# Performance work log

Hardware: AMD Instinct MI355X
Metric: run time of the kernel (lower is better)

The kernel has to match this reference:

```python
import jax, jax.numpy as jnp
import numpy as np

D_MODEL = 1024
NHEAD = 16


def unitnorm(v):
    # F.normalize(v, dim=-1): v / max(||v||_2, 1e-12)
    n = jnp.sqrt(jnp.sum(v * v, axis=-1, keepdims=True))
    return v / jnp.maximum(n, 1e-12)


def setup_inputs() -> dict:
    key = jax.random.key(0)
    ks = jax.random.split(key, 14)
    d = D_MODEL
    sc = 1.0 / np.sqrt(d)
    inp = jax.random.normal(ks[0], (2048, 8, d), dtype=jnp.float32)
    def lin(kw, kb, out_dim):
        W = jax.random.uniform(kw, (out_dim, d), minval=-sc, maxval=sc, dtype=jnp.float32)
        b = jax.random.uniform(kb, (out_dim,), minval=-sc, maxval=sc, dtype=jnp.float32)
        return W, b
    Wq_w, Wq_b = lin(ks[1], ks[2], d)
    Wk_w, Wk_b = lin(ks[3], ks[4], d)
    Wv_w, Wv_b = lin(ks[5], ks[6], d)
    Wo_w, Wo_b = lin(ks[7], ks[8], d)
    Ww_w, Ww_b = lin(ks[9], ks[10], NHEAD)
    Wr_w, Wr_b = lin(ks[11], ks[12], NHEAD)
    return {"inp": inp, "Wq_w": Wq_w, "Wq_b": Wq_b, "Wk_w": Wk_w, "Wk_b": Wk_b,
            "Wv_w": Wv_w, "Wv_b": Wv_b, "Wo_w": Wo_w, "Wo_b": Wo_b,
            "Ww_w": Ww_w, "Ww_b": Ww_b, "Wr_w": Wr_w, "Wr_b": Wr_b}


def reference(inp, Wq_w, Wq_b, Wk_w, Wk_b, Wv_w, Wv_b, Wo_w, Wo_b, Ww_w, Ww_b, Wr_w, Wr_b):
    src = inp  # src=None path
    S, B, d = inp.shape
    n = NHEAD
    # torch Linear: x @ W.T + b
    k = (src @ Wk_w.T + Wk_b).reshape(S, B, n, -1)
    v = (src @ Wv_w.T + Wv_b).reshape(S, B, n, -1)
    q = (inp @ Wq_w.T + Wq_b).reshape(S, B, n, -1)
    k = unitnorm(k)
    q = unitnorm(q)
    w = jax.nn.sigmoid(src @ Ww_w.T + Ww_b)            # [S,B,n]
    A = jnp.einsum('sbnq,sbnv->bnvq', k, v * w[:, :, :, None])
    r = jax.nn.sigmoid(inp @ Wr_w.T + Wr_b)            # [S,B,n]
    out = jnp.einsum('sbnq,bnvq->sbnv', q, A) * r[:, :, :, None]
    out = out.reshape(S, B, d)
    out = out @ Wo_w.T + Wo_b
    return (out, A)
```

## Files before the change

### kernel.cpp

```cpp
#include <hip/hip_runtime.h>
#include <cstdint>
#include <cstddef>


typedef __bf16 bf16x8 __attribute__((ext_vector_type(8)));
typedef float  f32x4  __attribute__((ext_vector_type(4)));
typedef unsigned short u16x8 __attribute__((ext_vector_type(8)));
typedef unsigned short u16x4 __attribute__((ext_vector_type(4)));

#define ROWS 16384
#define DM   1024

__device__ __forceinline__ unsigned short f2bf(float f) {
  unsigned int u = __builtin_bit_cast(unsigned int, f);
  u += 0x7FFFu + ((u >> 16) & 1u);
  return (unsigned short)(u >> 16);
}
__device__ __forceinline__ float bf2f(unsigned short h) {
  unsigned int u = ((unsigned int)h) << 16;
  return __builtin_bit_cast(float, u);
}
__device__ __forceinline__ float sigm(float x) { return 1.0f / (1.0f + __expf(-x)); }

__device__ __forceinline__ void gload_lds16(const void* g, void* l) {
  __builtin_amdgcn_global_load_lds((__attribute__((address_space(1))) void*)(g),
                                   (__attribute__((address_space(3))) void*)(l),
                                   16, 0, 0);
}

__global__ __launch_bounds__(256) void k_cast_x(const float* __restrict__ X,
                                                unsigned short* __restrict__ Xb) {
  size_t i = ((size_t)blockIdx.x * 256 + threadIdx.x) * 8;
  f32x4 a = *(const f32x4*)(X + i);
  f32x4 b = *(const f32x4*)(X + i + 4);
  u16x8 o;
  o[0] = f2bf(a[0]); o[1] = f2bf(a[1]); o[2] = f2bf(a[2]); o[3] = f2bf(a[3]);
  o[4] = f2bf(b[0]); o[5] = f2bf(b[1]); o[6] = f2bf(b[2]); o[7] = f2bf(b[3]);
  *(u16x8*)(Xb + i) = o;
}

__global__ __launch_bounds__(256) void k_pack_w(
    const float* __restrict__ Wq, const float* __restrict__ Wk, const float* __restrict__ Wv,
    const float* __restrict__ Wo, const float* __restrict__ Ww, const float* __restrict__ Wr,
    const float* __restrict__ bq, const float* __restrict__ bk, const float* __restrict__ bv,
    const float* __restrict__ bw, const float* __restrict__ br,
    unsigned short* __restrict__ Wpack, float* __restrict__ biasP,
    unsigned short* __restrict__ WRw, float* __restrict__ biasWR,
    unsigned short* __restrict__ Wob) {
  int r = blockIdx.x, t = threadIdx.x;
  const float* src; float bias = 0.0f; unsigned short* dst; float* bdst;
  if (r < 1024)      { src = Wq + (size_t)r * DM;          bias = bq[r];        dst = Wpack + (size_t)r * DM;          bdst = biasP + r; }
  else if (r < 2048) { src = Wk + (size_t)(r - 1024) * DM; bias = bk[r - 1024]; dst = Wpack + (size_t)r * DM;          bdst = biasP + r; }
  else if (r < 3072) { src = Wv + (size_t)(r - 2048) * DM; bias = bv[r - 2048]; dst = Wpack + (size_t)r * DM;          bdst = biasP + r; }
  else if (r < 3088) { src = Ww + (size_t)(r - 3072) * DM; bias = bw[r - 3072]; dst = WRw + (size_t)(r - 3072) * DM;   bdst = biasWR + (r - 3072); }
  else if (r < 3104) { src = Wr + (size_t)(r - 3088) * DM; bias = br[r - 3088]; dst = WRw + (size_t)(r - 3072) * DM;   bdst = biasWR + (r - 3072); }
  else               { src = Wo + (size_t)(r - 3104) * DM;                      dst = Wob + (size_t)(r - 3104) * DM;   bdst = nullptr; }
  int c = t * 4;
  f32x4 v = *(const f32x4*)(src + c);
  u16x4 o;
  o[0] = f2bf(v[0]); o[1] = f2bf(v[1]); o[2] = f2bf(v[2]); o[3] = f2bf(v[3]);
  *(u16x4*)(dst + c) = o;
  if (t == 0 && bdst) *bdst = bias;
}

__global__ __launch_bounds__(256) void k_wr(const unsigned short* __restrict__ Xb,
                                            const unsigned short* __restrict__ WRw,
                                            const float* __restrict__ biasWR,
                                            float* __restrict__ WRf) {
  __shared__ __bf16 sA[128 * 64];
  __shared__ __bf16 sB[32 * 64];
  int t = threadIdx.x, lane = t & 63, wid = t >> 6;
  int m0 = blockIdx.x * 128;
  int l15 = lane & 15, l4 = lane >> 4;
  f32x4 acc[2][2];
#pragma unroll
  for (int i = 0; i < 2; ++i)
#pragma unroll
    for (int j = 0; j < 2; ++j) acc[i][j] = (f32x4){0.f, 0.f, 0.f, 0.f};
  int srow = t >> 3, schunk = (t & 7) * 8;
  for (int kt = 0; kt < DM; kt += 64) {
#pragma unroll
    for (int c = 0; c < 4; ++c)
      gload_lds16(Xb + (size_t)(m0 + c * 32 + srow) * DM + kt + schunk,
                  (void*)(sA + c * 2048 + wid * 512));
    gload_lds16(WRw + (size_t)srow * DM + kt + schunk, (void*)(sB + wid * 512));
    __syncthreads();
#pragma unroll
    for (int ks = 0; ks < 2; ++ks) {
      bf16x8 fa[2], fb[2];
#pragma unroll
      for (int mi = 0; mi < 2; ++mi)
        fa[mi] = *(const bf16x8*)(sA + (wid * 32 + mi * 16 + l15) * 64 + (ks * 4 + l4) * 8);
#pragma unroll
      for (int ni = 0; ni < 2; ++ni)
        fb[ni] = *(const bf16x8*)(sB + (ni * 16 + l15) * 64 + (ks * 4 + l4) * 8);
#pragma unroll
      for (int mi = 0; mi < 2; ++mi)
#pragma unroll
        for (int ni = 0; ni < 2; ++ni)
          acc[mi][ni] = __builtin_amdgcn_mfma_f32_16x16x32_bf16(fa[mi], fb[ni], acc[mi][ni], 0, 0, 0);
    }
    __syncthreads();
  }
#pragma unroll
  for (int mi = 0; mi < 2; ++mi)
#pragma unroll
    for (int e = 0; e < 4; ++e) {
      int row = m0 + wid * 32 + mi * 16 + 4 * l4 + e;
#pragma unroll
      for (int ni = 0; ni < 2; ++ni)
        WRf[(size_t)row * 32 + ni * 16 + l15] = acc[mi][ni][e] + biasWR[ni * 16 + l15];
    }
}


#define VMW(N)  asm volatile("s_waitcnt vmcnt(" #N ")" ::: "memory")
#define LGKM(N) asm volatile("s_waitcnt lgkmcnt(" #N ")" ::: "memory")
#define SB0     __builtin_amdgcn_sched_barrier(0)

__device__ __forceinline__ void stageT(const unsigned short* __restrict__ Asrc,
                                       const unsigned short* __restrict__ Bsrc,
                                       int kt, __bf16* sm, int sb, int w) {
#pragma unroll
  for (int c = 0; c < 2; ++c)
    gload_lds16(Asrc + (size_t)c * 128 * DM + kt, (void*)(sm + sb + c * 4096 + w * 512));
#pragma unroll
  for (int c = 0; c < 2; ++c)
    gload_lds16(Bsrc + (size_t)c * 128 * DM + kt, (void*)(sm + sb + 8192 + c * 4096 + w * 512));
}

__device__ __forceinline__ void rdFA(bf16x8 (&fa)[8], const __bf16* base, const int (&aoff)[8]) {
#pragma unroll
  for (int mi = 0; mi < 8; ++mi) fa[mi] = *(const bf16x8*)(base + aoff[mi]);
}
__device__ __forceinline__ void rdFB(bf16x8 (&fb)[4], const __bf16* base, const int (&boff)[4]) {
#pragma unroll
  for (int ni = 0; ni < 4; ++ni) fb[ni] = *(const bf16x8*)(base + boff[ni]);
}

#define MFMA32(FB)                                                                   \
  do {                                                                               \
    __builtin_amdgcn_s_setprio(1);                                                   \
    _Pragma("unroll") for (int mi = 0; mi < 8; ++mi)                                 \
    _Pragma("unroll") for (int ni = 0; ni < 4; ++ni)                                 \
      acc[mi][ni] = __builtin_amdgcn_mfma_f32_16x16x32_bf16(fa[mi], FB[ni],          \
                                                            acc[mi][ni], 0, 0, 0);  \
    __builtin_amdgcn_s_setprio(0);                                                   \
    SB0;                                                                             \
  } while (0)

__device__ __forceinline__ void gemm_d4(const unsigned short* __restrict__ Ag,
                                        const unsigned short* __restrict__ Bg,
                                        __bf16* sm, f32x4 (&acc)[8][4],
                                        int m0, int n0, int lane, int w) {
  const int wm = w >> 2, wn = w & 3;
  const int l15 = lane & 15, l4 = lane >> 4;
  const int t = w * 64 + lane;
  const int srow = t >> 2;
  const int schunk = ((t & 3) ^ ((srow >> 1) & 3)) * 8;
  const unsigned short* Asrc = Ag + (size_t)(m0 + srow) * DM + schunk;
  const unsigned short* Bsrc = Bg + (size_t)(n0 + srow) * DM + schunk;

  int aoff[8], boff[4];
#pragma unroll
  for (int mi = 0; mi < 8; ++mi) {
    int r = wm * 128 + mi * 16 + l15;
    aoff[mi] = r * 32 + ((l4 ^ ((r >> 1) & 3)) << 3);
  }
#pragma unroll
  for (int ni = 0; ni < 4; ++ni) {
    int r = wn * 64 + ni * 16 + l15;
    boff[ni] = 8192 + r * 32 + ((l4 ^ ((r >> 1) & 3)) << 3);
  }

  bf16x8 fa[8], fbA[4], fbB[4];
  stageT(Asrc, Bsrc, 0,  sm, 0,     w);
  stageT(Asrc, Bsrc, 32, sm, 16384, w);
  stageT(Asrc, Bsrc, 64, sm, 32768, w);
  VMW(8);
  __builtin_amdgcn_s_barrier(); SB0;
  rdFB(fbA, sm, boff);
  rdFA(fa, sm, aoff);
  VMW(4);
  __builtin_amdgcn_s_barrier(); SB0;

  int sb = 49152;
  int rb = 16384;
  for (int i = 0; i < 14; ++i) {
    stageT(Asrc, Bsrc, (2 * i + 3) * 32, sm, sb, w); sb = (sb + 16384) & 65535;
    rdFB(fbB, sm + rb, boff);
    LGKM(4); SB0;
    MFMA32(fbA);
    rdFA(fa, sm + rb, aoff); rb = (rb + 16384) & 65535;
    VMW(4);
    __builtin_amdgcn_s_barrier(); SB0;
    stageT(Asrc, Bsrc, (2 * i + 4) * 32, sm, sb, w); sb = (sb + 16384) & 65535;
    rdFB(fbA, sm + rb, boff);
    LGKM(4); SB0;
    MFMA32(fbB);
    rdFA(fa, sm + rb, aoff); rb = (rb + 16384) & 65535;
    VMW(4);
    __builtin_amdgcn_s_barrier(); SB0;
  }
  stageT(Asrc, Bsrc, 992, sm, sb, w);
  rdFB(fbB, sm + rb, boff);
  LGKM(4); SB0;
  MFMA32(fbA);
  rdFA(fa, sm + rb, aoff); rb = (rb + 16384) & 65535;
  VMW(4);
  __builtin_amdgcn_s_barrier(); SB0;
  rdFB(fbA, sm + rb, boff);
  LGKM(4); SB0;
  MFMA32(fbB);
  rdFA(fa, sm + rb, aoff); rb = (rb + 16384) & 65535;
  VMW(0);
  __builtin_amdgcn_s_barrier(); SB0;
  rdFB(fbB, sm + rb, boff);
  LGKM(4); SB0;
  MFMA32(fbA);
  rdFA(fa, sm + rb, aoff);
  LGKM(0); SB0;
  MFMA32(fbB);
}

__global__ __launch_bounds__(512, 2) void k_gemm_qkv6(
    const unsigned short* __restrict__ Xb, const unsigned short* __restrict__ Wpack,
    const float* __restrict__ biasP, const float* __restrict__ WRf,
    unsigned short* __restrict__ Qb, unsigned short* __restrict__ Kb,
    unsigned short* __restrict__ Vb) {
  __shared__ __bf16 sm[65536];
  const int t = threadIdx.x, lane = t & 63, w = t >> 6;
  const int wm = w >> 2, wn = w & 3;
  const int l15 = lane & 15, l4 = lane >> 4;
  int orig = blockIdx.x;
  int wg = (orig & 7) * 96 + (orig >> 3);
  const int m0 = (wg & 63) << 8;
  const int n0 = (wg >> 6) << 8;
  f32x4 acc[8][4];
#pragma unroll
  for (int i = 0; i < 8; ++i)
#pragma unroll
    for (int j = 0; j < 4; ++j) acc[i][j] = (f32x4){0.f, 0.f, 0.f, 0.f};
  gemm_d4(Xb, Wpack, sm, acc, m0, n0, lane, w);

  const int colbase = n0 + wn * 64;
  float bb[4];
#pragma unroll
  for (int ni = 0; ni < 4; ++ni) bb[ni] = biasP[colbase + ni * 16 + l15];

  if (colbase < 2048) {
    unsigned short* dstp = (colbase < 1024) ? Qb : Kb;
    int coff = (colbase < 1024) ? colbase : (colbase - 1024);
#pragma unroll
    for (int mi = 0; mi < 8; ++mi)
#pragma unroll
      for (int e = 0; e < 4; ++e) {
        float v[4]; float ssq = 0.f;
#pragma unroll
        for (int ni = 0; ni < 4; ++ni) { v[ni] = acc[mi][ni][e] + bb[ni]; ssq += v[ni] * v[ni]; }
        ssq += __shfl_xor(ssq, 1);
        ssq += __shfl_xor(ssq, 2);
        ssq += __shfl_xor(ssq, 4);
        ssq += __shfl_xor(ssq, 8);
        float sc = 1.0f / fmaxf(sqrtf(ssq), 1e-12f);
        int row = m0 + wm * 128 + mi * 16 + 4 * l4 + e;
#pragma unroll
        for (int ni = 0; ni < 4; ++ni)
          dstp[(size_t)row * DM + coff + ni * 16 + l15] = f2bf(v[ni] * sc);
      }
  } else {
    int hv = (colbase - 2048) >> 6;
    int coff = colbase - 2048;
#pragma unroll
    for (int mi = 0; mi < 8; ++mi)
#pragma unroll
      for (int e = 0; e < 4; ++e) {
        int row = m0 + wm * 128 + mi * 16 + 4 * l4 + e;
        float wgt = sigm(WRf[(size_t)row * 32 + hv]);
#pragma unroll
        for (int ni = 0; ni < 4; ++ni)
          Vb[(size_t)row * DM + coff + ni * 16 + l15] = f2bf((acc[mi][ni][e] + bb[ni]) * wgt);
      }
  }
}

__global__ __launch_bounds__(512, 2) void k_gemm_out6(
    const unsigned short* __restrict__ Ob, const unsigned short* __restrict__ Wob,
    const float* __restrict__ bo, float* __restrict__ Out) {
  __shared__ __bf16 sm[65536];
  const int t = threadIdx.x, lane = t & 63, w = t >> 6;
  const int wm = w >> 2, wn = w & 3;
  const int l15 = lane & 15, l4 = lane >> 4;
  int orig = blockIdx.x;
  int wg = (orig & 7) * 32 + (orig >> 3);
  const int m0 = (wg & 63) << 8;
  const int n0 = (wg >> 6) << 8;
  f32x4 acc[8][4];
#pragma unroll
  for (int i = 0; i < 8; ++i)
#pragma unroll
    for (int j = 0; j < 4; ++j) acc[i][j] = (f32x4){0.f, 0.f, 0.f, 0.f};
  gemm_d4(Ob, Wob, sm, acc, m0, n0, lane, w);

  float bb[4];
#pragma unroll
  for (int ni = 0; ni < 4; ++ni) bb[ni] = bo[n0 + wn * 64 + ni * 16 + l15];
#pragma unroll
  for (int mi = 0; mi < 8; ++mi)
#pragma unroll
    for (int e = 0; e < 4; ++e) {
      int row = m0 + wm * 128 + mi * 16 + 4 * l4 + e;
#pragma unroll
      for (int ni = 0; ni < 4; ++ni) {
        int col = n0 + wn * 64 + ni * 16 + l15;
        Out[(size_t)row * DM + col] = acc[mi][ni][e] + bb[ni];
      }
    }
}

__global__ __launch_bounds__(256, 2) void k_gemm_A(const unsigned short* __restrict__ Kb,
                                                   const unsigned short* __restrict__ Vb,
                                                   float* __restrict__ Apart) {
  __shared__ __bf16 sK[64 * 64];
  __shared__ __bf16 sV[64 * 64];
  int t = threadIdx.x, lane = t & 63, wid = t >> 6;
  int bn = blockIdx.x & 127, sk = blockIdx.x >> 7;
  int b = bn >> 4, n = bn & 15;
  f32x4 acc[4];
#pragma unroll
  for (int j = 0; j < 4; j++) acc[j] = (f32x4){0.f, 0.f, 0.f, 0.f};
  int lrow = lane >> 3, lcol = (lane & 7) * 8;

  for (int st = sk * 1024; st < (sk + 1) * 1024; st += 64) {
#pragma unroll
    for (int c = 0; c < 2; c++) {
      int r0 = wid * 16 + c * 8;
      size_t g = ((size_t)(st + r0 + lrow) * 8 + b) * DM + n * 64 + lcol;
      gload_lds16(Kb + g, (void*)(sK + r0 * 64));
      gload_lds16(Vb + g, (void*)(sV + r0 * 64));
    }
    __syncthreads();
#pragma unroll
    for (int kk = 0; kk < 64; kk += 32) {
      bf16x8 av, bv[4];
#pragma unroll
      for (int e = 0; e < 8; e++)
        av[e] = sV[(kk + 8 * (lane >> 4) + e) * 64 + wid * 16 + (lane & 15)];
#pragma unroll
      for (int jn = 0; jn < 4; jn++)
#pragma unroll
        for (int e = 0; e < 8; e++)
          bv[jn][e] = sK[(kk + 8 * (lane >> 4) + e) * 64 + jn * 16 + (lane & 15)];
#pragma unroll
      for (int jn = 0; jn < 4; jn++)
        acc[jn] = __builtin_amdgcn_mfma_f32_16x16x32_bf16(av, bv[jn], acc[jn], 0, 0, 0);
    }
    __syncthreads();
  }
  float* Ap = Apart + (size_t)(sk * 128 + bn) * 4096;
#pragma unroll
  for (int jn = 0; jn < 4; jn++) {
#pragma unroll
    for (int e = 0; e < 4; e++) {
      int i = wid * 16 + 4 * (lane >> 4) + e;
      int j = jn * 16 + (lane & 15);
      Ap[i * 64 + j] = acc[jn][e];
    }
  }
}

__global__ __launch_bounds__(256) void k_reduceA(const float* __restrict__ Apart,
                                                 float* __restrict__ Aout,
                                                 unsigned short* __restrict__ Abf) {
  int bn = blockIdx.x, t = threadIdx.x;
  size_t base = (size_t)bn * 4096 + t * 16;
#pragma unroll
  for (int j = 0; j < 4; ++j) {
    f32x4 x = *(const f32x4*)(Apart + base + j * 4);
    f32x4 y = *(const f32x4*)(Apart + (size_t)128 * 4096 + base + j * 4);
    x += y;
    *(f32x4*)(Aout + base + j * 4) = x;
    u16x4 o;
    o[0] = f2bf(x[0]); o[1] = f2bf(x[1]); o[2] = f2bf(x[2]); o[3] = f2bf(x[3]);
    *(u16x4*)(Abf + base + j * 4) = o;
  }
}

__global__ __launch_bounds__(256, 2) void k_gemm_o2(const unsigned short* __restrict__ Qb,
                                                    const unsigned short* __restrict__ Abf,
                                                    const float* __restrict__ WRf,
                                                    unsigned short* __restrict__ Ob) {
  __shared__ __bf16 sQ[128 * 64];
  __shared__ __bf16 sA[64 * 64];
  int t = threadIdx.x, lane = t & 63, wid = t >> 6;
  int bn = blockIdx.x & 127, stile = blockIdx.x >> 7;
  int b = bn >> 4, n = bn & 15;
  int s0 = stile * 128;
  int lrow = lane >> 3, lcol = (lane & 7) * 8;
#pragma unroll
  for (int c = 0; c < 4; c++) {
    int r0 = wid * 32 + c * 8;
    gload_lds16(Qb + ((size_t)(s0 + r0 + lrow) * 8 + b) * DM + n * 64 + lcol,
                (void*)(sQ + r0 * 64));
  }
#pragma unroll
  for (int c = 0; c < 2; c++) {
    int r0 = wid * 16 + c * 8;
    gload_lds16(Abf + (size_t)bn * 4096 + (size_t)(r0 + lrow) * 64 + lcol,
                (void*)(sA + r0 * 64));
  }
  __syncthreads();
  f32x4 acc[2][4];
#pragma unroll
  for (int i = 0; i < 2; i++)
#pragma unroll
    for (int j = 0; j < 4; j++) acc[i][j] = (f32x4){0.f, 0.f, 0.f, 0.f};
#pragma unroll
  for (int kk = 0; kk < 64; kk += 32) {
    bf16x8 aq[2], bA[4];
#pragma unroll
    for (int mi = 0; mi < 2; mi++)
      aq[mi] = *(const bf16x8*)(sQ + (wid * 32 + mi * 16 + (lane & 15)) * 64 + kk + 8 * (lane >> 4));
#pragma unroll
    for (int ni = 0; ni < 4; ni++)
      bA[ni] = *(const bf16x8*)(sA + (ni * 16 + (lane & 15)) * 64 + kk + 8 * (lane >> 4));
#pragma unroll
    for (int mi = 0; mi < 2; mi++)
#pragma unroll
      for (int ni = 0; ni < 4; ni++)
        acc[mi][ni] = __builtin_amdgcn_mfma_f32_16x16x32_bf16(aq[mi], bA[ni], acc[mi][ni], 0, 0, 0);
  }
#pragma unroll
  for (int mi = 0; mi < 2; mi++) {
#pragma unroll
    for (int e = 0; e < 4; e++) {
      int srow = wid * 32 + mi * 16 + 4 * (lane >> 4) + e;
      size_t row = (size_t)(s0 + srow) * 8 + b;
      float rv = sigm(WRf[row * 32 + 16 + n]);
#pragma unroll
      for (int ni = 0; ni < 4; ni++)
        Ob[row * DM + n * 64 + ni * 16 + (lane & 15)] = f2bf(acc[mi][ni][e] * rv);
    }
  }
}

extern "C" void kernel_launch(void* const* d_in, const int* in_sizes, int n_in,
                              void* d_out, int out_size, void* d_ws, size_t ws_size,
                              hipStream_t stream) {
  (void)in_sizes; (void)n_in; (void)out_size; (void)ws_size;
  const float* X  = (const float*)d_in[0];
  const float* Wq = (const float*)d_in[1];  const float* bq = (const float*)d_in[2];
  const float* Wk = (const float*)d_in[3];  const float* bk = (const float*)d_in[4];
  const float* Wv = (const float*)d_in[5];  const float* bv = (const float*)d_in[6];
  const float* Wo = (const float*)d_in[7];  const float* bo = (const float*)d_in[8];
  const float* Ww = (const float*)d_in[9];  const float* bw = (const float*)d_in[10];
  const float* Wr = (const float*)d_in[11]; const float* br = (const float*)d_in[12];

  char* ws = (char*)d_ws;
  unsigned short* Wpack = (unsigned short*)(ws + 0);
  float*          Apart = (float*)(ws + 0);
  unsigned short* Abf   = (unsigned short*)(ws + 4194304);
  float*          biasP = (float*)(ws + 6291456);
  unsigned short* WRw   = (unsigned short*)(ws + 6303744);
  float*          biasWR= (float*)(ws + 6369280);
  unsigned short* Wob   = (unsigned short*)(ws + 6369408);
  unsigned short* Xb    = (unsigned short*)(ws + 8466560);
  unsigned short* Ob    = Xb;
  unsigned short* Qb    = (unsigned short*)(ws + 42020992);
  unsigned short* Kb    = (unsigned short*)(ws + 75575424);
  unsigned short* Vb    = (unsigned short*)(ws + 109129856);
  float*          WRf   = (float*)(ws + 142684288);

  float* Out0 = (float*)d_out;
  float* Aout = Out0 + (size_t)ROWS * DM;

  k_cast_x<<<dim3(8192), dim3(256), 0, stream>>>(X, Xb);
  k_pack_w<<<dim3(4128), dim3(256), 0, stream>>>(Wq, Wk, Wv, Wo, Ww, Wr,
                                                 bq, bk, bv, bw, br,
                                                 Wpack, biasP, WRw, biasWR, Wob);
  k_wr<<<dim3(128), dim3(256), 0, stream>>>(Xb, WRw, biasWR, WRf);
  k_gemm_qkv6<<<dim3(768), dim3(512), 0, stream>>>(Xb, Wpack, biasP, WRf, Qb, Kb, Vb);
  k_gemm_A<<<dim3(256), dim3(256), 0, stream>>>(Kb, Vb, Apart);
  k_reduceA<<<dim3(128), dim3(256), 0, stream>>>(Apart, Aout, Abf);
  k_gemm_o2<<<dim3(2048), dim3(256), 0, stream>>>(Qb, Abf, WRf, Ob);
  k_gemm_out6<<<dim3(256), dim3(512), 0, stream>>>(Ob, Wob, bo, Out0);
}
```

Before: 241.9 us.

## Fuse X cast into k_wr, replace QKV GEMM pipeline, add nontemporal stores

Removes the separate fp32-to-bf16 cast kernel. k_wr now reads fp32 X directly, converts it, writes Xb to global and stages it into LDS for its own GEMM. Replaces the hand-pipelined QKV GEMM (gemm_d4 with explicit waitcnt scheduling) with a simpler double-buffered 64-wide K loop that uses XOR-swizzled LDS layout. Switches output stores in several kernels to nontemporal. This saves a launch and one pass over X, but k_wr runs only 128 blocks and now carries the whole cast, and the simpler GEMM loop may overlap loads with compute less well than the tuned one.

```diff
diff --git a/kernel.cpp b/kernel.cpp
--- a/kernel.cpp
+++ b/kernel.cpp
@@ -26,17 +26,6 @@
   __builtin_amdgcn_global_load_lds((__attribute__((address_space(1))) void*)(g),
                                    (__attribute__((address_space(3))) void*)(l),
                                    16, 0, 0);
-}
-
-__global__ __launch_bounds__(256) void k_cast_x(const float* __restrict__ X,
-                                                unsigned short* __restrict__ Xb) {
-  size_t i = ((size_t)blockIdx.x * 256 + threadIdx.x) * 8;
-  f32x4 a = *(const f32x4*)(X + i);
-  f32x4 b = *(const f32x4*)(X + i + 4);
-  u16x8 o;
-  o[0] = f2bf(a[0]); o[1] = f2bf(a[1]); o[2] = f2bf(a[2]); o[3] = f2bf(a[3]);
-  o[4] = f2bf(b[0]); o[5] = f2bf(b[1]); o[6] = f2bf(b[2]); o[7] = f2bf(b[3]);
-  *(u16x8*)(Xb + i) = o;
 }
 
 __global__ __launch_bounds__(256) void k_pack_w(
@@ -63,9 +52,10 @@
   if (t == 0 && bdst) *bdst = bias;
 }
 
-__global__ __launch_bounds__(256) void k_wr(const unsigned short* __restrict__ Xb,
+__global__ __launch_bounds__(256) void k_wr(const float* __restrict__ X,
                                             const unsigned short* __restrict__ WRw,
                                             const float* __restrict__ biasWR,
+                                            unsigned short* __restrict__ Xb,
                                             float* __restrict__ WRf) {
   __shared__ __bf16 sA[128 * 64];
   __shared__ __bf16 sB[32 * 64];
@@ -78,12 +68,24 @@
 #pragma unroll
     for (int j = 0; j < 2; ++j) acc[i][j] = (f32x4){0.f, 0.f, 0.f, 0.f};
   int srow = t >> 3, schunk = (t & 7) * 8;
+  int xr = t >> 1, xc = (t & 1) * 32;
   for (int kt = 0; kt < DM; kt += 64) {
-#pragma unroll
-    for (int c = 0; c < 4; ++c)
-      gload_lds16(Xb + (size_t)(m0 + c * 32 + srow) * DM + kt + schunk,
-                  (void*)(sA + c * 2048 + wid * 512));
     gload_lds16(WRw + (size_t)srow * DM + kt + schunk, (void*)(sB + wid * 512));
+    const float* xsrc = X + (size_t)(m0 + xr) * DM + kt + xc;
+    f32x4 xv[8];
+#pragma unroll
+    for (int j = 0; j < 8; ++j) xv[j] = *(const f32x4*)(xsrc + j * 4);
+    u16x8 o[4];
+#pragma unroll
+    for (int j = 0; j < 4; ++j) {
+#pragma unroll
+      for (int e = 0; e < 4; ++e) {
+        o[j][e]     = f2bf(xv[2 * j][e]);
+        o[j][e + 4] = f2bf(xv[2 * j + 1][e]);
+      }
+      *(u16x8*)(Xb + (size_t)(m0 + xr) * DM + kt + xc + j * 8) = o[j];
+      *(u16x8*)((unsigned short*)(sA + xr * 64 + xc) + j * 8) = o[j];
+    }
     __syncthreads();
 #pragma unroll
     for (int ks = 0; ks < 2; ++ks) {
@@ -113,6 +115,110 @@
     }
 }
 
+__global__ __launch_bounds__(512, 2) void k_gemm_qkv7(
+    const unsigned short* __restrict__ Xb, const unsigned short* __restrict__ Wpack,
+    const float* __restrict__ biasP, const float* __restrict__ WRf,
+    unsigned short* __restrict__ Qb, unsigned short* __restrict__ Kb,
+    unsigned short* __restrict__ Vb) {
+  __shared__ __bf16 sm[65536];
+  const int t = threadIdx.x, lane = t & 63, w = t >> 6;
+  const int wm = w >> 2, wn = w & 3;
+  const int l15 = lane & 15, l4 = lane >> 4, l7 = lane & 7;
+  int orig = blockIdx.x;
+  int wg = (orig & 7) * 96 + (orig >> 3);
+  const int m0 = (wg & 63) << 8;
+  const int n0 = (wg >> 6) << 8;
+
+  const int srow = t >> 3;
+  const int schunk = ((t & 7) ^ (srow & 7)) * 8;
+  const unsigned short* Asrc = Xb + (size_t)(m0 + srow) * DM + schunk;
+  const unsigned short* Bsrc = Wpack + (size_t)(n0 + srow) * DM + schunk;
+
+  f32x4 acc[8][4];
+#pragma unroll
+  for (int i = 0; i < 8; ++i)
+#pragma unroll
+    for (int j = 0; j < 4; ++j) acc[i][j] = (f32x4){0.f, 0.f, 0.f, 0.f};
+
+#define STAGE256(P, kt)                                                            \
+  do {                                                                             \
+    _Pragma("unroll") for (int c = 0; c < 4; ++c)                                  \
+      gload_lds16(Asrc + (size_t)c * 64 * DM + (kt),                               \
+                  (void*)(sm + (P) * 32768 + c * 4096 + w * 512));                 \
+    _Pragma("unroll") for (int c = 0; c < 4; ++c)                                  \
+      gload_lds16(Bsrc + (size_t)c * 64 * DM + (kt),                               \
+                  (void*)(sm + (P) * 32768 + 16384 + c * 4096 + w * 512));         \
+  } while (0)
+
+  STAGE256(0, 0);
+  __syncthreads();
+  for (int kt16 = 0; kt16 < 16; ++kt16) {
+    int P = kt16 & 1;
+    if (kt16 < 15) STAGE256(P ^ 1, (kt16 + 1) * 64);
+    const __bf16* A0 = sm + P * 32768;
+    const __bf16* B0 = A0 + 16384;
+#pragma unroll
+    for (int ks = 0; ks < 2; ++ks) {
+      bf16x8 fa[8], fb[4];
+      int ck = (((ks * 4 + l4) ^ l7) << 3);
+#pragma unroll
+      for (int mi = 0; mi < 8; ++mi)
+        fa[mi] = *(const bf16x8*)(A0 + (wm * 128 + mi * 16 + l15) * 64 + ck);
+#pragma unroll
+      for (int ni = 0; ni < 4; ++ni)
+        fb[ni] = *(const bf16x8*)(B0 + (wn * 64 + ni * 16 + l15) * 64 + ck);
+#pragma unroll
+      for (int mi = 0; mi < 8; ++mi)
+#pragma unroll
+        for (int ni = 0; ni < 4; ++ni)
+          acc[mi][ni] = __builtin_amdgcn_mfma_f32_16x16x32_bf16(fa[mi], fb[ni], acc[mi][ni], 0, 0, 0);
+    }
+    __syncthreads();
+  }
+#undef STAGE256
+
+  const int colbase = n0 + wn * 64;
+  float bb[4];
+#pragma unroll
+  for (int ni = 0; ni < 4; ++ni) bb[ni] = biasP[colbase + ni * 16 + l15];
+
+  if (colbase < 2048) {
+    unsigned short* dstp = (colbase < 1024) ? Qb : Kb;
+    int coff = (colbase < 1024) ? colbase : (colbase - 1024);
+#pragma unroll
+    for (int mi = 0; mi < 8; ++mi)
+#pragma unroll
+      for (int e = 0; e < 4; ++e) {
+        float v[4]; float ssq = 0.f;
+#pragma unroll
+        for (int ni = 0; ni < 4; ++ni) { v[ni] = acc[mi][ni][e] + bb[ni]; ssq += v[ni] * v[ni]; }
+        ssq += __shfl_xor(ssq, 1);
+        ssq += __shfl_xor(ssq, 2);
+        ssq += __shfl_xor(ssq, 4);
+        ssq += __shfl_xor(ssq, 8);
+        float sc = 1.0f / fmaxf(sqrtf(ssq), 1e-12f);
+        int row = m0 + wm * 128 + mi * 16 + 4 * l4 + e;
+#pragma unroll
+        for (int ni = 0; ni < 4; ++ni)
+          __builtin_nontemporal_store(f2bf(v[ni] * sc),
+                                      &dstp[(size_t)row * DM + coff + ni * 16 + l15]);
+      }
+  } else {
+    int hv = (colbase - 2048) >> 6;
+    int coff = colbase - 2048;
+#pragma unroll
+    for (int mi = 0; mi < 8; ++mi)
+#pragma unroll
+      for (int e = 0; e < 4; ++e) {
+        int row = m0 + wm * 128 + mi * 16 + 4 * l4 + e;
+        float wgt = sigm(WRf[(size_t)row * 32 + hv]);
+#pragma unroll
+        for (int ni = 0; ni < 4; ++ni)
+          __builtin_nontemporal_store(f2bf((acc[mi][ni][e] + bb[ni]) * wgt),
+                                      &Vb[(size_t)row * DM + coff + ni * 16 + l15]);
+      }
+  }
+}
 
 #define VMW(N)  asm volatile("s_waitcnt vmcnt(" #N ")" ::: "memory")
 #define LGKM(N) asm volatile("s_waitcnt lgkmcnt(" #N ")" ::: "memory")
@@ -223,68 +329,7 @@
   MFMA32(fbB);
 }
 
-__global__ __launch_bounds__(512, 2) void k_gemm_qkv6(
-    const unsigned short* __restrict__ Xb, const unsigned short* __restrict__ Wpack,
-    const float* __restrict__ biasP, const float* __restrict__ WRf,
-    unsigned short* __restrict__ Qb, unsigned short* __restrict__ Kb,
-    unsigned short* __restrict__ Vb) {
-  __shared__ __bf16 sm[65536];
-  const int t = threadIdx.x, lane = t & 63, w = t >> 6;
-  const int wm = w >> 2, wn = w & 3;
-  const int l15 = lane & 15, l4 = lane >> 4;
-  int orig = blockIdx.x;
-  int wg = (orig & 7) * 96 + (orig >> 3);
-  const int m0 = (wg & 63) << 8;
-  const int n0 = (wg >> 6) << 8;
-  f32x4 acc[8][4];
-#pragma unroll
-  for (int i = 0; i < 8; ++i)
-#pragma unroll
-    for (int j = 0; j < 4; ++j) acc[i][j] = (f32x4){0.f, 0.f, 0.f, 0.f};
-  gemm_d4(Xb, Wpack, sm, acc, m0, n0, lane, w);
-
-  const int colbase = n0 + wn * 64;
-  float bb[4];
-#pragma unroll
-  for (int ni = 0; ni < 4; ++ni) bb[ni] = biasP[colbase + ni * 16 + l15];
-
-  if (colbase < 2048) {
-    unsigned short* dstp = (colbase < 1024) ? Qb : Kb;
-    int coff = (colbase < 1024) ? colbase : (colbase - 1024);
-#pragma unroll
-    for (int mi = 0; mi < 8; ++mi)
-#pragma unroll
-      for (int e = 0; e < 4; ++e) {
-        float v[4]; float ssq = 0.f;
-#pragma unroll
-        for (int ni = 0; ni < 4; ++ni) { v[ni] = acc[mi][ni][e] + bb[ni]; ssq += v[ni] * v[ni]; }
-        ssq += __shfl_xor(ssq, 1);
-        ssq += __shfl_xor(ssq, 2);
-        ssq += __shfl_xor(ssq, 4);
-        ssq += __shfl_xor(ssq, 8);
-        float sc = 1.0f / fmaxf(sqrtf(ssq), 1e-12f);
-        int row = m0 + wm * 128 + mi * 16 + 4 * l4 + e;
-#pragma unroll
-        for (int ni = 0; ni < 4; ++ni)
-          dstp[(size_t)row * DM + coff + ni * 16 + l15] = f2bf(v[ni] * sc);
-      }
-  } else {
-    int hv = (colbase - 2048) >> 6;
-    int coff = colbase - 2048;
-#pragma unroll
-    for (int mi = 0; mi < 8; ++mi)
-#pragma unroll
-      for (int e = 0; e < 4; ++e) {
-        int row = m0 + wm * 128 + mi * 16 + 4 * l4 + e;
-        float wgt = sigm(WRf[(size_t)row * 32 + hv]);
-#pragma unroll
-        for (int ni = 0; ni < 4; ++ni)
-          Vb[(size_t)row * DM + coff + ni * 16 + l15] = f2bf((acc[mi][ni][e] + bb[ni]) * wgt);
-      }
-  }
-}
-
-__global__ __launch_bounds__(512, 2) void k_gemm_out6(
+__global__ __launch_bounds__(512, 2) void k_gemm_out7(
     const unsigned short* __restrict__ Ob, const unsigned short* __restrict__ Wob,
     const float* __restrict__ bo, float* __restrict__ Out) {
   __shared__ __bf16 sm[65536];
@@ -313,7 +358,7 @@
 #pragma unroll
       for (int ni = 0; ni < 4; ++ni) {
         int col = n0 + wn * 64 + ni * 16 + l15;
-        Out[(size_t)row * DM + col] = acc[mi][ni][e] + bb[ni];
+        __builtin_nontemporal_store(acc[mi][ni][e] + bb[ni], &Out[(size_t)row * DM + col]);
       }
     }
 }
@@ -379,7 +424,10 @@
     f32x4 x = *(const f32x4*)(Apart + base + j * 4);
     f32x4 y = *(const f32x4*)(Apart + (size_t)128 * 4096 + base + j * 4);
     x += y;
-    *(f32x4*)(Aout + base + j * 4) = x;
+    __builtin_nontemporal_store(x[0], Aout + base + j * 4 + 0);
+    __builtin_nontemporal_store(x[1], Aout + base + j * 4 + 1);
+    __builtin_nontemporal_store(x[2], Aout + base + j * 4 + 2);
+    __builtin_nontemporal_store(x[3], Aout + base + j * 4 + 3);
     u16x4 o;
     o[0] = f2bf(x[0]); o[1] = f2bf(x[1]); o[2] = f2bf(x[2]); o[3] = f2bf(x[3]);
     *(u16x4*)(Abf + base + j * 4) = o;
@@ -474,14 +522,13 @@
   float* Out0 = (float*)d_out;
   float* Aout = Out0 + (size_t)ROWS * DM;
 
-  k_cast_x<<<dim3(8192), dim3(256), 0, stream>>>(X, Xb);
   k_pack_w<<<dim3(4128), dim3(256), 0, stream>>>(Wq, Wk, Wv, Wo, Ww, Wr,
                                                  bq, bk, bv, bw, br,
                                                  Wpack, biasP, WRw, biasWR, Wob);
-  k_wr<<<dim3(128), dim3(256), 0, stream>>>(Xb, WRw, biasWR, WRf);
-  k_gemm_qkv6<<<dim3(768), dim3(512), 0, stream>>>(Xb, Wpack, biasP, WRf, Qb, Kb, Vb);
+  k_wr<<<dim3(128), dim3(256), 0, stream>>>(X, WRw, biasWR, Xb, WRf);
+  k_gemm_qkv7<<<dim3(768), dim3(512), 0, stream>>>(Xb, Wpack, biasP, WRf, Qb, Kb, Vb);
   k_gemm_A<<<dim3(256), dim3(256), 0, stream>>>(Kb, Vb, Apart);
   k_reduceA<<<dim3(128), dim3(256), 0, stream>>>(Apart, Aout, Abf);
   k_gemm_o2<<<dim3(2048), dim3(256), 0, stream>>>(Qb, Abf, WRf, Ob);
-  k_gemm_out6<<<dim3(256), dim3(512), 0, stream>>>(Ob, Wob, bo, Out0);
-}
+  k_gemm_out7<<<dim3(256), dim3(512), 0, stream>>>(Ob, Wob, bo, Out0);
+}
```

New measurement: 264.0 us. 9.2% more time.
